# Performance work log

Measured on AMD Instinct MI355X. Metric: run time of the kernel, lower is better.

The kernel has to match this reference:

```python
import jax, jax.numpy as jnp
import numpy as np

HIDDEN_DIM = 64
VOCAB_SIZE = 128
NUM_SLOTS = 64
B, L = 256, 4096


def layer_norm(x, gamma, beta, eps=1e-5):
    mu = jnp.mean(x, axis=-1, keepdims=True)
    var = jnp.mean(jnp.square(x - mu), axis=-1, keepdims=True)
    return (x - mu) * jax.lax.rsqrt(var + eps) * gamma + beta


def _l2norm(x, axis=-1, eps=1e-12):
    # matches torch F.normalize: x / max(||x||, eps)
    n = jnp.sqrt(jnp.sum(jnp.square(x), axis=axis, keepdims=True))
    return x / jnp.maximum(n, eps)


def setup_inputs() -> dict:
    key = jax.random.key(0)
    ks = jax.random.split(key, 13)
    H, V, S = HIDDEN_DIM, VOCAB_SIZE, NUM_SLOTS
    return {
        "seq": jax.random.randint(ks[0], (B, L), 0, V),
        "embed_w": jax.random.normal(ks[1], (V, H), dtype=jnp.float32),
        # linear weights stored [in, out] (transposed vs torch)
        "w1": jax.random.normal(ks[2], (H, 2 * H), dtype=jnp.float32) * 0.05,
        "b1": jnp.zeros((2 * H,), dtype=jnp.float32),
        "w2": jax.random.normal(ks[3], (2 * H, H), dtype=jnp.float32) * 0.05,
        "b2": jnp.zeros((H,), dtype=jnp.float32),
        "ln_g": jnp.ones((H,), dtype=jnp.float32),
        "ln_b": jnp.zeros((H,), dtype=jnp.float32),
        "slot_keys": jax.random.normal(ks[4], (S, H), dtype=jnp.float32) * 0.1,
        "slot_vals": jax.random.normal(ks[5], (S, H), dtype=jnp.float32) * 0.1,
        "gate_w": jax.random.normal(ks[6], (H, S), dtype=jnp.float32) * 0.05,
        "gate_b": jnp.zeros((S,), dtype=jnp.float32),
        "out_w": jax.random.normal(ks[7], (H, V), dtype=jnp.float32) * 0.05,
        "out_b": jnp.zeros((V,), dtype=jnp.float32),
    }


def reference(seq, embed_w, w1, b1, w2, b2, ln_g, ln_b,
              slot_keys, slot_vals, gate_w, gate_b, out_w, out_b):
    h = embed_w[seq]                                   # [B, L, H]
    ff = jnp.maximum(h @ w1 + b1, 0.0) @ w2 + b2       # [B, L, H]
    h = layer_norm(h + ff, ln_g, ln_b)

    hw = h[:, :-1, :]                                  # written tokens [B, L-1, H]
    w = jax.nn.softmax(hw @ gate_w + gate_b, axis=-1)  # [B, L-1, S]
    # the per-step increment w_t (outer) h_t is independent of prior keys,
    # so the sequential loop collapses exactly to one contraction:
    keys = slot_keys[None, :, :] + jnp.einsum('btn,bth->bnh', w, hw)  # [B, S, H]
    vals = keys  # loop sets vals = keys every step; L > 1 here

    q = h[:, -1, :]                                    # [B, H]
    sim = jnp.einsum('bnh,bh->bn', _l2norm(keys), _l2norm(q))
    attn = jax.nn.softmax(sim, axis=-1)                # [B, S]
    ctx = jnp.einsum('bn,bnh->bh', attn, vals)         # [B, H]
    return ctx @ out_w + out_b                         # [B, V]
```

## Files before the change

kernel.cpp:

```cpp
#include <hip/hip_runtime.h>

#define HD 64
#define VC 128
#define NS 64
#define NB 256
#define SL 4096

typedef __attribute__((ext_vector_type(8))) short short8;
typedef __attribute__((ext_vector_type(4))) float f32x4;

#define SWZ(row, col_u) ((((row) * VC) + (col_u)) ^ (((row) & 7) << 3))

__device__ __forceinline__ float wsum(float x) {
#pragma unroll
  for (int o = 32; o > 0; o >>= 1) x += __shfl_xor(x, o, 64);
  return x;
}
__device__ __forceinline__ float wmax(float x) {
#pragma unroll
  for (int o = 32; o > 0; o >>= 1) x = fmaxf(x, __shfl_xor(x, o, 64));
  return x;
}

__global__ __launch_bounds__(128) void build_tables(
    const float* __restrict__ embed, const float* __restrict__ w1, const float* __restrict__ b1,
    const float* __restrict__ w2, const float* __restrict__ b2,
    const float* __restrict__ ln_g, const float* __restrict__ ln_b,
    const float* __restrict__ gate_w, const float* __restrict__ gate_b,
    float* __restrict__ HN, float* __restrict__ WSM)
{
  const int v = blockIdx.x, t = threadIdx.x;
  __shared__ float s_e[HD], s_f1[2 * HD], s_hn[HD], s_red[128];

  if (t < HD) s_e[t] = embed[v * HD + t];
  __syncthreads();

  {
    float a0 = 0.f, a1 = 0.f, a2 = 0.f, a3 = 0.f;
#pragma unroll
    for (int h = 0; h < HD; h += 4) {
      a0 = fmaf(s_e[h + 0], w1[(h + 0) * 2 * HD + t], a0);
      a1 = fmaf(s_e[h + 1], w1[(h + 1) * 2 * HD + t], a1);
      a2 = fmaf(s_e[h + 2], w1[(h + 2) * 2 * HD + t], a2);
      a3 = fmaf(s_e[h + 3], w1[(h + 3) * 2 * HD + t], a3);
    }
    s_f1[t] = fmaxf(b1[t] + ((a0 + a1) + (a2 + a3)), 0.f);
  }
  __syncthreads();

  {
    const int col = t & 63;
    const int j0 = (t >> 6) << 6;
    float a0 = 0.f, a1 = 0.f, a2 = 0.f, a3 = 0.f;
#pragma unroll
    for (int j = 0; j < 64; j += 4) {
      a0 = fmaf(s_f1[j0 + j + 0], w2[(j0 + j + 0) * HD + col], a0);
      a1 = fmaf(s_f1[j0 + j + 1], w2[(j0 + j + 1) * HD + col], a1);
      a2 = fmaf(s_f1[j0 + j + 2], w2[(j0 + j + 2) * HD + col], a2);
      a3 = fmaf(s_f1[j0 + j + 3], w2[(j0 + j + 3) * HD + col], a3);
    }
    s_red[t] = (a0 + a1) + (a2 + a3);
  }
  __syncthreads();

  if (t < HD) {
    float x = s_e[t] + b2[t] + s_red[t] + s_red[t + 64];
    float mu = wsum(x) * (1.f / 64.f);
    float d = x - mu;
    float var = wsum(d * d) * (1.f / 64.f);
    float hn = d * rsqrtf(var + 1e-5f) * ln_g[t] + ln_b[t];
    s_hn[t] = hn;
    HN[v * HD + t] = hn;
  }
  __syncthreads();

  {
    const int col = t & 63;
    const int hh0 = (t >> 6) << 5;
    float a0 = 0.f, a1 = 0.f, a2 = 0.f, a3 = 0.f;
#pragma unroll
    for (int h = 0; h < 32; h += 4) {
      a0 = fmaf(s_hn[hh0 + h + 0], gate_w[(hh0 + h + 0) * NS + col], a0);
      a1 = fmaf(s_hn[hh0 + h + 1], gate_w[(hh0 + h + 1) * NS + col], a1);
      a2 = fmaf(s_hn[hh0 + h + 2], gate_w[(hh0 + h + 2) * NS + col], a2);
      a3 = fmaf(s_hn[hh0 + h + 3], gate_w[(hh0 + h + 3) * NS + col], a3);
    }
    s_red[t] = (a0 + a1) + (a2 + a3);
  }
  __syncthreads();

  if (t < NS) {
    float g = gate_b[t] + s_red[t] + s_red[t + 64];
    float m = wmax(g);
    float e = expf(g - m);
    float s = wsum(e);
    WSM[v * NS + t] = e / s;
  }
}

__global__ __launch_bounds__(1024) void batch_kernel(
    const int* __restrict__ seq, const float* __restrict__ HN, const float* __restrict__ WSM,
    const float* __restrict__ slot_keys, const float* __restrict__ out_w,
    const float* __restrict__ out_b, float* __restrict__ out)
{
  const int b = blockIdx.x, t = threadIdx.x;
  const int lane = t & 63, wave = t >> 6;

  __shared__ int s_cnt[VC];
  __shared__ int s_qtok;
  __align__(16) __shared__ unsigned short s_wt_hi[NS * VC];
  __align__(16) __shared__ unsigned short s_wt_lo[NS * VC];
  __align__(16) __shared__ unsigned short s_ht_hi[HD * VC];
  __align__(16) __shared__ unsigned short s_ht_lo[HD * VC];
  __align__(16) __shared__ float s_keys[NS * HD];
  __align__(16) __shared__ float s_part[16 * HD];
  __shared__ float s_q[HD], s_sim[NS], s_ctx[HD];

  const int col64 = t & 63;
  const int vb = t >> 6;

  const int n0 = (wave & 3) << 4;
  const int h0 = (wave >> 2) << 4;
  const int fr = lane & 15;
  const int fg = lane >> 4;

  const int* sb = seq + b * SL;
  const int4 sv = ((const int4*)sb)[t];

  float wreg[8], hreg[8];
#pragma unroll
  for (int j = 0; j < 8; ++j) {
    wreg[j] = WSM[(vb * 8 + j) * NS + col64];
    hreg[j] = HN[(vb * 8 + j) * HD + col64];
  }
  float skv[4];
#pragma unroll
  for (int r = 0; r < 4; ++r)
    skv[r] = slot_keys[(n0 + fg * 4 + r) * HD + h0 + fr];

  if (t < VC) s_cnt[t] = 0;
  __syncthreads();

  atomicAdd(&s_cnt[sv.x], 1);
  atomicAdd(&s_cnt[sv.y], 1);
  atomicAdd(&s_cnt[sv.z], 1);
  if (t != 1023) atomicAdd(&s_cnt[sv.w], 1);
  else s_qtok = sv.w;
  __syncthreads();

  {
    short8 vwhi, vwlo, vhhi, vhlo;
#pragma unroll
    for (int j = 0; j < 8; ++j) {
      const float c = (float)s_cnt[vb * 8 + j];
      const float w = wreg[j] * c;
      const unsigned int wb_ = __float_as_uint(w);
      vwhi[j] = (short)(wb_ >> 16);
      const float wr = w - __uint_as_float(wb_ & 0xffff0000u);
      vwlo[j] = (short)(__float_as_uint(wr) >> 16);

      const float h = hreg[j];
      const unsigned int hb_ = __float_as_uint(h);
      vhhi[j] = (short)(hb_ >> 16);
      const float hr = h - __uint_as_float(hb_ & 0xffff0000u);
      vhlo[j] = (short)(__float_as_uint(hr) >> 16);
    }
    const int idx = SWZ(col64, vb * 8);
    *(short8*)&s_wt_hi[idx] = vwhi;
    *(short8*)&s_wt_lo[idx] = vwlo;
    *(short8*)&s_ht_hi[idx] = vhhi;
    *(short8*)&s_ht_lo[idx] = vhlo;
  }
  {
    const int qtok = s_qtok;
    if (vb == (qtok >> 3)) {
      const int qj = qtok & 7;
      float qv = hreg[0];
#pragma unroll
      for (int j = 1; j < 8; ++j) if (qj == j) qv = hreg[j];
      s_q[col64] = qv;
    }
  }
  __syncthreads();

  {
    f32x4 acc = {skv[0], skv[1], skv[2], skv[3]};
#pragma unroll
    for (int kc = 0; kc < 4; ++kc) {
      const int au = SWZ(n0 + fr, fg * 8 + kc * 32);
      const int bu = SWZ(h0 + fr, fg * 8 + kc * 32);
      const short8 ahi = *(const short8*)&s_wt_hi[au];
      const short8 alo = *(const short8*)&s_wt_lo[au];
      const short8 bhi = *(const short8*)&s_ht_hi[bu];
      const short8 blo = *(const short8*)&s_ht_lo[bu];
      acc = __builtin_amdgcn_mfma_f32_16x16x32_bf16(ahi, bhi, acc, 0, 0, 0);
      acc = __builtin_amdgcn_mfma_f32_16x16x32_bf16(ahi, blo, acc, 0, 0, 0);
      acc = __builtin_amdgcn_mfma_f32_16x16x32_bf16(alo, bhi, acc, 0, 0, 0);
      acc = __builtin_amdgcn_mfma_f32_16x16x32_bf16(alo, blo, acc, 0, 0, 0);
    }
#pragma unroll
    for (int r = 0; r < 4; ++r)
      s_keys[(n0 + fg * 4 + r) * HD + h0 + fr] = acc[r];
  }
  __syncthreads();

  const float qv = s_q[lane];
  const float qn = fmaxf(sqrtf(wsum(qv * qv)), 1e-12f);
#pragma unroll
  for (int r = 0; r < 4; ++r) {
    const int n = (wave << 2) + r;
    const float kv = s_keys[n * HD + lane];
    const float kk = wsum(kv * kv);
    const float kq = wsum(kv * qv);
    if (lane == 0) s_sim[n] = kq / (fmaxf(sqrtf(kk), 1e-12f) * qn);
  }
  __syncthreads();

  {
    const float svv = s_sim[lane];
    const float m = wmax(svv);
    const float e = expf(svv - m);
    const float ssum = wsum(e);
    const float attn_l = e / ssum;
    float c = 0.f;
#pragma unroll
    for (int r = 0; r < 4; ++r) {
      const int n = (wave << 2) + r;
      const float an = __shfl(attn_l, n, 64);
      c = fmaf(an, s_keys[n * HD + lane], c);
    }
    s_part[wave * HD + lane] = c;
  }
  __syncthreads();
  if (wave == 0) {
    float c0 = 0.f, c1 = 0.f, c2 = 0.f, c3 = 0.f;
#pragma unroll
    for (int w = 0; w < 16; w += 4) {
      c0 += s_part[(w + 0) * HD + lane];
      c1 += s_part[(w + 1) * HD + lane];
      c2 += s_part[(w + 2) * HD + lane];
      c3 += s_part[(w + 3) * HD + lane];
    }
    s_ctx[lane] = (c0 + c1) + (c2 + c3);
  }
  __syncthreads();

  if (t < VC) {
    float o0 = 0.f, o1 = 0.f, o2 = 0.f, o3 = 0.f;
#pragma unroll
    for (int h = 0; h < HD; h += 4) {
      o0 = fmaf(s_ctx[h + 0], out_w[(h + 0) * VC + t], o0);
      o1 = fmaf(s_ctx[h + 1], out_w[(h + 1) * VC + t], o1);
      o2 = fmaf(s_ctx[h + 2], out_w[(h + 2) * VC + t], o2);
      o3 = fmaf(s_ctx[h + 3], out_w[(h + 3) * VC + t], o3);
    }
    out[b * VC + t] = out_b[t] + ((o0 + o1) + (o2 + o3));
  }
}

extern "C" void kernel_launch(void* const* d_in, const int* in_sizes, int n_in,
                              void* d_out, int out_size, void* d_ws, size_t ws_size,
                              hipStream_t stream) {
  const int* seq         = (const int*)d_in[0];
  const float* embed_w   = (const float*)d_in[1];
  const float* w1        = (const float*)d_in[2];
  const float* b1        = (const float*)d_in[3];
  const float* w2        = (const float*)d_in[4];
  const float* b2        = (const float*)d_in[5];
  const float* ln_g      = (const float*)d_in[6];
  const float* ln_b      = (const float*)d_in[7];
  const float* slot_keys = (const float*)d_in[8];
  const float* gate_w    = (const float*)d_in[10];
  const float* gate_b    = (const float*)d_in[11];
  const float* out_w     = (const float*)d_in[12];
  const float* out_b     = (const float*)d_in[13];
  float* out = (float*)d_out;

  float* HN  = (float*)d_ws;
  float* WSM = HN + VC * HD;

  build_tables<<<VC, 128, 0, stream>>>(embed_w, w1, b1, w2, b2, ln_g, ln_b,
                                       gate_w, gate_b, HN, WSM);
  batch_kernel<<<NB, 1024, 0, stream>>>(seq, HN, WSM, slot_keys, out_w, out_b, out);
}
```

Before: 92.05 us.

## Precompute swizzled bf16 hi/lo hidden table and transposed gate softmax in setup kernel

The table-building kernel now writes the normalized hidden table already split into bf16 hi/lo halves in the swizzled LDS layout, and stores the gate softmax transposed. Each batch block can then copy the hidden table straight into shared memory with vector loads, and only the count-scaled weight split is done per block. This removes redundant per-block conversion of the hidden table and uses wider coalesced loads. The output projection weights are also prefetched into shared memory early, so their global latency overlaps the histogram phase, at the cost of 32KB more LDS per block.

```diff
diff --git a/kernel.cpp b/kernel.cpp
--- a/kernel.cpp
+++ b/kernel.cpp
@@ -27,7 +27,8 @@
     const float* __restrict__ w2, const float* __restrict__ b2,
     const float* __restrict__ ln_g, const float* __restrict__ ln_b,
     const float* __restrict__ gate_w, const float* __restrict__ gate_b,
-    float* __restrict__ HN, float* __restrict__ WSM)
+    float* __restrict__ WSMT, unsigned short* __restrict__ HtHi,
+    unsigned short* __restrict__ HtLo)
 {
   const int v = blockIdx.x, t = threadIdx.x;
   __shared__ float s_e[HD], s_f1[2 * HD], s_hn[HD], s_red[128];
@@ -70,7 +71,13 @@
     float var = wsum(d * d) * (1.f / 64.f);
     float hn = d * rsqrtf(var + 1e-5f) * ln_g[t] + ln_b[t];
     s_hn[t] = hn;
-    HN[v * HD + t] = hn;
+    const unsigned int hb_ = __float_as_uint(hn);
+    const unsigned short hi = (unsigned short)(hb_ >> 16);
+    const float rem = hn - __uint_as_float(hb_ & 0xffff0000u);
+    const unsigned short lo = (unsigned short)(__float_as_uint(rem) >> 16);
+    const int idx = SWZ(t, v);
+    HtHi[idx] = hi;
+    HtLo[idx] = lo;
   }
   __syncthreads();
 
@@ -94,12 +101,13 @@
     float m = wmax(g);
     float e = expf(g - m);
     float s = wsum(e);
-    WSM[v * NS + t] = e / s;
+    WSMT[t * VC + v] = e / s;
   }
 }
 
 __global__ __launch_bounds__(1024) void batch_kernel(
-    const int* __restrict__ seq, const float* __restrict__ HN, const float* __restrict__ WSM,
+    const int* __restrict__ seq, const float* __restrict__ WSMT,
+    const unsigned short* __restrict__ HtHi, const unsigned short* __restrict__ HtLo,
     const float* __restrict__ slot_keys, const float* __restrict__ out_w,
     const float* __restrict__ out_b, float* __restrict__ out)
 {
@@ -112,27 +120,27 @@
   __align__(16) __shared__ unsigned short s_wt_lo[NS * VC];
   __align__(16) __shared__ unsigned short s_ht_hi[HD * VC];
   __align__(16) __shared__ unsigned short s_ht_lo[HD * VC];
+  __align__(16) __shared__ float s_ow[HD * VC];
   __align__(16) __shared__ float s_keys[NS * HD];
   __align__(16) __shared__ float s_part[16 * HD];
   __shared__ float s_q[HD], s_sim[NS], s_ctx[HD];
 
-  const int col64 = t & 63;
-  const int vb = t >> 6;
+  const int wn = t >> 4;
+  const int wv8 = (t & 15) << 3;
 
   const int n0 = (wave & 3) << 4;
   const int h0 = (wave >> 2) << 4;
   const int fr = lane & 15;
   const int fg = lane >> 4;
 
-  const int* sb = seq + b * SL;
-  const int4 sv = ((const int4*)sb)[t];
-
-  float wreg[8], hreg[8];
-#pragma unroll
-  for (int j = 0; j < 8; ++j) {
-    wreg[j] = WSM[(vb * 8 + j) * NS + col64];
-    hreg[j] = HN[(vb * 8 + j) * HD + col64];
-  }
+  const int4 sv = ((const int4*)(seq + b * SL))[t];
+  const float4 wt0 = *(const float4*)&WSMT[wn * VC + wv8];
+  const float4 wt1 = *(const float4*)&WSMT[wn * VC + wv8 + 4];
+  const short8 hhi = ((const short8*)HtHi)[t];
+  const short8 hlo = ((const short8*)HtLo)[t];
+  const float4 ow0 = ((const float4*)out_w)[t];
+  const float4 ow1 = ((const float4*)out_w)[t + 1024];
+  const float ob = (t < VC) ? out_b[t] : 0.f;
   float skv[4];
 #pragma unroll
   for (int r = 0; r < 4; ++r)
@@ -146,40 +154,35 @@
   atomicAdd(&s_cnt[sv.z], 1);
   if (t != 1023) atomicAdd(&s_cnt[sv.w], 1);
   else s_qtok = sv.w;
-  __syncthreads();
-
-  {
-    short8 vwhi, vwlo, vhhi, vhlo;
+  ((short8*)s_ht_hi)[t] = hhi;
+  ((short8*)s_ht_lo)[t] = hlo;
+  ((float4*)s_ow)[t] = ow0;
+  ((float4*)s_ow)[t + 1024] = ow1;
+  __syncthreads();
+
+  {
+    const int4 c0 = *(const int4*)&s_cnt[wv8];
+    const int4 c1 = *(const int4*)&s_cnt[wv8 + 4];
+    float wf[8] = {wt0.x, wt0.y, wt0.z, wt0.w, wt1.x, wt1.y, wt1.z, wt1.w};
+    const int cc[8] = {c0.x, c0.y, c0.z, c0.w, c1.x, c1.y, c1.z, c1.w};
+    short8 vhi, vlo;
 #pragma unroll
     for (int j = 0; j < 8; ++j) {
-      const float c = (float)s_cnt[vb * 8 + j];
-      const float w = wreg[j] * c;
+      const float w = wf[j] * (float)cc[j];
       const unsigned int wb_ = __float_as_uint(w);
-      vwhi[j] = (short)(wb_ >> 16);
+      vhi[j] = (short)(wb_ >> 16);
       const float wr = w - __uint_as_float(wb_ & 0xffff0000u);
-      vwlo[j] = (short)(__float_as_uint(wr) >> 16);
-
-      const float h = hreg[j];
-      const unsigned int hb_ = __float_as_uint(h);
-      vhhi[j] = (short)(hb_ >> 16);
-      const float hr = h - __uint_as_float(hb_ & 0xffff0000u);
-      vhlo[j] = (short)(__float_as_uint(hr) >> 16);
-    }
-    const int idx = SWZ(col64, vb * 8);
-    *(short8*)&s_wt_hi[idx] = vwhi;
-    *(short8*)&s_wt_lo[idx] = vwlo;
-    *(short8*)&s_ht_hi[idx] = vhhi;
-    *(short8*)&s_ht_lo[idx] = vhlo;
-  }
-  {
+      vlo[j] = (short)(__float_as_uint(wr) >> 16);
+    }
+    const int idx = SWZ(wn, wv8);
+    *(short8*)&s_wt_hi[idx] = vhi;
+    *(short8*)&s_wt_lo[idx] = vlo;
+  }
+  if (t < HD) {
     const int qtok = s_qtok;
-    if (vb == (qtok >> 3)) {
-      const int qj = qtok & 7;
-      float qv = hreg[0];
-#pragma unroll
-      for (int j = 1; j < 8; ++j) if (qj == j) qv = hreg[j];
-      s_q[col64] = qv;
-    }
+    const unsigned int hi = s_ht_hi[SWZ(t, qtok)];
+    const unsigned int lo = s_ht_lo[SWZ(t, qtok)];
+    s_q[t] = __uint_as_float(hi << 16) + __uint_as_float(lo << 16);
   }
   __syncthreads();
 
@@ -249,12 +252,12 @@
     float o0 = 0.f, o1 = 0.f, o2 = 0.f, o3 = 0.f;
 #pragma unroll
     for (int h = 0; h < HD; h += 4) {
-      o0 = fmaf(s_ctx[h + 0], out_w[(h + 0) * VC + t], o0);
-      o1 = fmaf(s_ctx[h + 1], out_w[(h + 1) * VC + t], o1);
-      o2 = fmaf(s_ctx[h + 2], out_w[(h + 2) * VC + t], o2);
-      o3 = fmaf(s_ctx[h + 3], out_w[(h + 3) * VC + t], o3);
-    }
-    out[b * VC + t] = out_b[t] + ((o0 + o1) + (o2 + o3));
+      o0 = fmaf(s_ctx[h + 0], s_ow[(h + 0) * VC + t], o0);
+      o1 = fmaf(s_ctx[h + 1], s_ow[(h + 1) * VC + t], o1);
+      o2 = fmaf(s_ctx[h + 2], s_ow[(h + 2) * VC + t], o2);
+      o3 = fmaf(s_ctx[h + 3], s_ow[(h + 3) * VC + t], o3);
+    }
+    out[b * VC + t] = ob + ((o0 + o1) + (o2 + o3));
   }
 }
 
@@ -276,10 +279,12 @@
   const float* out_b     = (const float*)d_in[13];
   float* out = (float*)d_out;
 
-  float* HN  = (float*)d_ws;
-  float* WSM = HN + VC * HD;
+  float* WSMT = (float*)d_ws;
+  unsigned short* HtHi = (unsigned short*)(WSMT + NS * VC);
+  unsigned short* HtLo = HtHi + HD * VC;
 
   build_tables<<<VC, 128, 0, stream>>>(embed_w, w1, b1, w2, b2, ln_g, ln_b,
-                                       gate_w, gate_b, HN, WSM);
-  batch_kernel<<<NB, 1024, 0, stream>>>(seq, HN, WSM, slot_keys, out_w, out_b, out);
-}
+                                       gate_w, gate_b, WSMT, HtHi, HtLo);
+  batch_kernel<<<NB, 1024, 0, stream>>>(seq, WSMT, HtHi, HtLo, slot_keys,
+                                        out_w, out_b, out);
+}
```

Measured after the change: 92.02 us. Within noise of the previous version (-0.0%).
